# Kernel tuning notes

Hardware: AMD Instinct MI355X
Metric: run time of the kernel (lower is better)

Reference implementation:

```python
import jax, jax.numpy as jnp
import numpy as np

C1 = 256
C2 = 256
C = 256

def setup_inputs() -> dict:
    key = jax.random.key(0)
    ks = jax.random.split(key, 8)
    B, S, H, W = 4, 8, 32, 32
    img_feat = jax.random.normal(ks[0], (B, S, C1, H, W), dtype=jnp.float32)
    depth_feat = jax.random.normal(ks[1], (B, S, C2, H, W), dtype=jnp.float32)
    sq = 1.0 / np.sqrt(C1)
    sk = 1.0 / np.sqrt(C2)
    Wq = jax.random.uniform(ks[2], (C1, C), jnp.float32, -sq, sq)
    bq = jax.random.uniform(ks[3], (C,), jnp.float32, -sq, sq)
    Wk = jax.random.uniform(ks[4], (C2, C), jnp.float32, -sk, sk)
    bk = jax.random.uniform(ks[5], (C,), jnp.float32, -sk, sk)
    Wv = jax.random.uniform(ks[6], (C2, C), jnp.float32, -sk, sk)
    bv = jax.random.uniform(ks[7], (C,), jnp.float32, -sk, sk)
    return {"img_feat": img_feat, "depth_feat": depth_feat,
            "Wq": Wq, "bq": bq, "Wk": Wk, "bk": bk, "Wv": Wv, "bv": bv}

def reference(img_feat, depth_feat, Wq, bq, Wk, bk, Wv, bv):
    B, S, _, H, W = img_feat.shape
    hw = H * W
    # channels-last, flatten spatial: [B,S,hw,c1]
    img = jnp.transpose(img_feat, (0, 1, 3, 4, 2)).reshape(B, S, hw, -1)
    depth = jnp.transpose(depth_feat, (0, 1, 3, 4, 2)).reshape(B, S, hw, -1)
    q = (img @ Wq + bq).astype(jnp.float32)    # [B,S,hw,c]
    k = (depth @ Wk + bk).astype(jnp.float32)  # [B,S,hw,c]
    v = (depth @ Wv + bv).astype(jnp.float32)  # [B,S,hw,c]
    scale = 1.0 / jnp.sqrt(jnp.float32(Wq.shape[1]))
    scores = jnp.einsum('bsqc,bskc->bsqk', q, k) * scale  # [B,S,hw,hw]
    attn = jax.nn.softmax(scores, axis=-1)
    out = jnp.einsum('bsqk,bskc->bsqc', attn, v)          # [B,S,hw,c]
    out = out + img                                        # residual (c == c1)
    out = out.reshape(B, S, H, W, -1).astype(img_feat.dtype)
    return jnp.transpose(out, (0, 1, 4, 2, 3))             # [B,S,c,H,W]
```

## Files before the change

kernel.cpp:

```cpp
#include <hip/hip_runtime.h>
#include <hip/hip_bf16.h>

typedef __hip_bfloat16 bf16;
typedef __attribute__((ext_vector_type(8))) short short8v;
typedef __attribute__((ext_vector_type(4))) float f32x4;

#define NSLICE 32
#define HW     1024
#define CDIM   256
#define KVT    32

__global__ __launch_bounds__(256)
void wt_prep_kernel(const float* __restrict__ Wq, const float* __restrict__ Wk,
                    const float* __restrict__ Wv, bf16* __restrict__ wt)
{
    const int m = blockIdx.x >> 8;
    const int r = blockIdx.x & 255;
    const int tid = threadIdx.x;
    const float* W = (m == 0) ? Wq : (m == 1) ? Wk : Wv;
    const float sc = (m == 0) ? 0.0625f : 1.0f;
    wt[((size_t)m << 16) + (size_t)tid * 256 + r] = __float2bfloat16(W[r * 256 + tid] * sc);
}

__global__ __launch_bounds__(256)
void qkv_mfma_kernel(const float* __restrict__ img, const float* __restrict__ dep,
                     const bf16* __restrict__ wt,
                     const float* __restrict__ bq, const float* __restrict__ bk,
                     const float* __restrict__ bv,
                     bf16* __restrict__ qo, bf16* __restrict__ ko, bf16* __restrict__ vt)
{
    const int bid   = blockIdx.x;
    const int chalf = bid & 1;
    const int tt    = (bid >> 1) & 15;
    const int s     = bid >> 5;
    const int t0    = tt * 64;

    const int tid  = threadIdx.x;
    const int wave = tid >> 6;
    const int lane = tid & 63;
    const int lo16 = lane & 15;
    const int hi4  = lane >> 4;
    const int cw0  = chalf * 128 + wave * 32;

    __shared__ short Ai[64][40];
    __shared__ short Ad[64][40];

    const int so = tid >> 6;
    const int st = tid & 63;

    const float* imgS = img + (size_t)s * CDIM * HW + t0;
    const float* depS = dep + (size_t)s * CDIM * HW + t0;

    const bf16* wtq = wt;
    const bf16* wtk = wt + (1 << 16);
    const bf16* wtv = wt + (2 << 16);

    f32x4 aq[2][4], ak[2][4], av[4][2];
    #pragma unroll
    for (int a = 0; a < 2; ++a)
        #pragma unroll
        for (int b = 0; b < 4; ++b) {
            aq[a][b] = (f32x4){0.f, 0.f, 0.f, 0.f};
            ak[a][b] = (f32x4){0.f, 0.f, 0.f, 0.f};
            av[b][a] = (f32x4){0.f, 0.f, 0.f, 0.f};
        }

    float ri[8], rd[8];
    #pragma unroll
    for (int j = 0; j < 8; ++j) {
        ri[j] = imgS[(size_t)(so * 8 + j) * HW + st];
        rd[j] = depS[(size_t)(so * 8 + j) * HW + st];
    }

    for (int kc = 0; kc < 8; ++kc) {
        __syncthreads();
        {
            short ti[8], td[8];
            #pragma unroll
            for (int j = 0; j < 8; ++j) {
                bf16 hi = __float2bfloat16(ri[j]);
                bf16 hd = __float2bfloat16(rd[j]);
                ti[j] = *reinterpret_cast<short*>(&hi);
                td[j] = *reinterpret_cast<short*>(&hd);
            }
            *reinterpret_cast<short8v*>(&Ai[st][so * 8]) = *reinterpret_cast<short8v*>(ti);
            *reinterpret_cast<short8v*>(&Ad[st][so * 8]) = *reinterpret_cast<short8v*>(td);
        }
        __syncthreads();

        if (kc < 7) {
            #pragma unroll
            for (int j = 0; j < 8; ++j) {
                ri[j] = imgS[(size_t)((kc + 1) * 32 + so * 8 + j) * HW + st];
                rd[j] = depS[(size_t)((kc + 1) * 32 + so * 8 + j) * HW + st];
            }
        }

        short8v xi[4], xd[4];
        #pragma unroll
        for (int nf = 0; nf < 4; ++nf) {
            xi[nf] = *reinterpret_cast<const short8v*>(&Ai[nf * 16 + lo16][hi4 * 8]);
            xd[nf] = *reinterpret_cast<const short8v*>(&Ad[nf * 16 + lo16][hi4 * 8]);
        }
        const int koff = kc * 32 + hi4 * 8;
        short8v wqf[2], wkf[2], wvf[2];
        #pragma unroll
        for (int mf = 0; mf < 2; ++mf) {
            const size_t wrow = (size_t)(cw0 + mf * 16 + lo16) * 256 + koff;
            wqf[mf] = *reinterpret_cast<const short8v*>(wtq + wrow);
            wkf[mf] = *reinterpret_cast<const short8v*>(wtk + wrow);
            wvf[mf] = *reinterpret_cast<const short8v*>(wtv + wrow);
        }

        #pragma unroll
        for (int mf = 0; mf < 2; ++mf)
            #pragma unroll
            for (int nf = 0; nf < 4; ++nf) {
                aq[mf][nf] = __builtin_amdgcn_mfma_f32_16x16x32_bf16(wqf[mf], xi[nf], aq[mf][nf], 0, 0, 0);
                ak[mf][nf] = __builtin_amdgcn_mfma_f32_16x16x32_bf16(wkf[mf], xd[nf], ak[mf][nf], 0, 0, 0);
            }
        #pragma unroll
        for (int mf = 0; mf < 4; ++mf)
            #pragma unroll
            for (int nf = 0; nf < 2; ++nf)
                av[mf][nf] = __builtin_amdgcn_mfma_f32_16x16x32_bf16(xd[mf], wvf[nf], av[mf][nf], 0, 0, 0);
    }

    #pragma unroll
    for (int mf = 0; mf < 2; ++mf) {
        const int cb = cw0 + mf * 16 + 4 * hi4;
        const float4 b4q = *reinterpret_cast<const float4*>(bq + cb);
        const float4 b4k = *reinterpret_cast<const float4*>(bk + cb);
        const float bqa[4] = {b4q.x * 0.0625f, b4q.y * 0.0625f, b4q.z * 0.0625f, b4q.w * 0.0625f};
        const float bka[4] = {b4k.x, b4k.y, b4k.z, b4k.w};
        #pragma unroll
        for (int nf = 0; nf < 4; ++nf) {
            const int tok = t0 + nf * 16 + lo16;
            bf16 tq[4], tk[4];
            #pragma unroll
            for (int g = 0; g < 4; ++g) {
                tq[g] = __float2bfloat16(aq[mf][nf][g] + bqa[g]);
                tk[g] = __float2bfloat16(ak[mf][nf][g] + bka[g]);
            }
            const size_t base = ((size_t)s * HW + tok) * CDIM + cb;
            *reinterpret_cast<uint2*>(&qo[base]) = *reinterpret_cast<uint2*>(tq);
            *reinterpret_cast<uint2*>(&ko[base]) = *reinterpret_cast<uint2*>(tk);
        }
    }
    #pragma unroll
    for (int nf = 0; nf < 2; ++nf) {
        const int c = cw0 + nf * 16 + lo16;
        const float bvv = bv[c];
        #pragma unroll
        for (int mf = 0; mf < 4; ++mf) {
            const int tb = t0 + mf * 16 + 4 * hi4;
            bf16 tv[4];
            #pragma unroll
            for (int g = 0; g < 4; ++g)
                tv[g] = __float2bfloat16(av[mf][nf][g] + bvv);
            *reinterpret_cast<uint2*>(&vt[((size_t)s * CDIM + c) * HW + tb]) =
                *reinterpret_cast<uint2*>(tv);
        }
    }
}

__global__ __launch_bounds__(256)
void flash_mfma_kernel(const bf16* __restrict__ q, const bf16* __restrict__ k,
                       const bf16* __restrict__ vt, const float* __restrict__ img,
                       float* __restrict__ out)
{
    const int bid = blockIdx.x;
    const int qt  = bid >> 5;
    const int rr_ = bid & 31;
    const int s   = (rr_ & 7) * 4 + (rr_ >> 3);
    const int t0  = qt * 64;

    const int tid  = threadIdx.x;
    const int wave = tid >> 6;
    const int lane = tid & 63;
    const int lo16 = lane & 15;
    const int hi4  = lane >> 4;

    __shared__ short Ks[KVT][264];
    __shared__ short Vs[CDIM][36];
    __shared__ short Ps[4][16][36];

    short8v qf[8];
    {
        const int qrow = t0 + wave * 16 + lo16;
        const bf16* qp = q + ((size_t)s * HW + qrow) * CDIM + hi4 * 8;
        #pragma unroll
        for (int kf = 0; kf < 8; ++kf)
            qf[kf] = *reinterpret_cast<const short8v*>(qp + kf * 32);
    }

    f32x4 Oacc[16];
    #pragma unroll
    for (int cf = 0; cf < 16; ++cf) Oacc[cf] = (f32x4){0.f, 0.f, 0.f, 0.f};
    float lp[4] = {0.f, 0.f, 0.f, 0.f};

    const bf16* kS  = k  + (size_t)s * HW * CDIM;
    const bf16* vtS = vt + (size_t)s * CDIM * HW;

    const int krow = tid >> 3;
    const int kch  = tid & 7;
    const int vcl  = lane >> 2;
    const int vtq  = (lane & 3) * 8;

    short8v kreg[4], vreg[4];
    {
        #pragma unroll
        for (int u = 0; u < 4; ++u)
            kreg[u] = *reinterpret_cast<const short8v*>(kS + (size_t)krow * CDIM + (kch + u * 8) * 8);
        #pragma unroll
        for (int u = 0; u < 4; ++u) {
            const int c = wave * 64 + u * 16 + vcl;
            vreg[u] = *reinterpret_cast<const short8v*>(vtS + (size_t)c * HW + vtq);
        }
    }

    for (int kt = 0; kt < HW / KVT; ++kt) {
        __syncthreads();
        #pragma unroll
        for (int u = 0; u < 4; ++u)
            *reinterpret_cast<short8v*>(&Ks[krow][(kch + u * 8) * 8]) = kreg[u];
        #pragma unroll
        for (int u = 0; u < 4; ++u)
            *reinterpret_cast<short8v*>(&Vs[wave * 64 + u * 16 + vcl][vtq]) = vreg[u];
        __syncthreads();

        if (kt + 1 < HW / KVT) {
            const bf16* src = kS + (size_t)(kt + 1) * KVT * CDIM;
            #pragma unroll
            for (int u = 0; u < 4; ++u)
                kreg[u] = *reinterpret_cast<const short8v*>(src + (size_t)krow * CDIM + (kch + u * 8) * 8);
            #pragma unroll
            for (int u = 0; u < 4; ++u) {
                const int c = wave * 64 + u * 16 + vcl;
                vreg[u] = *reinterpret_cast<const short8v*>(vtS + (size_t)c * HW + (kt + 1) * KVT + vtq);
            }
        }

        f32x4 sa[2];
        sa[0] = (f32x4){0.f, 0.f, 0.f, 0.f};
        sa[1] = (f32x4){0.f, 0.f, 0.f, 0.f};
        __builtin_amdgcn_s_setprio(1);
        #pragma unroll
        for (int ks = 0; ks < 8; ++ks) {
            #pragma unroll
            for (int cf = 0; cf < 2; ++cf) {
                short8v bfr = *reinterpret_cast<const short8v*>(
                    &Ks[cf * 16 + lo16][ks * 32 + hi4 * 8]);
                sa[cf] = __builtin_amdgcn_mfma_f32_16x16x32_bf16(qf[ks], bfr, sa[cf], 0, 0, 0);
            }
        }
        __builtin_amdgcn_s_setprio(0);

        #pragma unroll
        for (int cf = 0; cf < 2; ++cf)
            #pragma unroll
            for (int g = 0; g < 4; ++g) {
                const float e = __expf(sa[cf][g]);
                lp[g] += e;
                bf16 hb = __float2bfloat16(e);
                Ps[wave][4 * hi4 + g][cf * 16 + lo16] = *reinterpret_cast<short*>(&hb);
            }

        const short8v pa = *reinterpret_cast<const short8v*>(&Ps[wave][lo16][hi4 * 8]);

        __builtin_amdgcn_s_setprio(1);
        #pragma unroll
        for (int cf = 0; cf < 16; ++cf) {
            const short8v vb = *reinterpret_cast<const short8v*>(&Vs[cf * 16 + lo16][hi4 * 8]);
            Oacc[cf] = __builtin_amdgcn_mfma_f32_16x16x32_bf16(pa, vb, Oacc[cf], 0, 0, 0);
        }
        __builtin_amdgcn_s_setprio(0);
    }

    float inv[4];
    #pragma unroll
    for (int g = 0; g < 4; ++g) {
        float l = lp[g];
        #pragma unroll
        for (int off = 1; off < 16; off <<= 1) l += __shfl_xor(l, off);
        inv[g] = 1.0f / l;
    }
    const float* imgS = img + (size_t)s * CDIM * HW;
    float*       outS = out + (size_t)s * CDIM * HW;
    const int tt = t0 + wave * 16 + 4 * hi4;
    #pragma unroll
    for (int cf = 0; cf < 16; ++cf) {
        const int c = cf * 16 + lo16;
        const float4 r4 = *reinterpret_cast<const float4*>(imgS + (size_t)c * HW + tt);
        float4 o;
        o.x = Oacc[cf][0] * inv[0] + r4.x;
        o.y = Oacc[cf][1] * inv[1] + r4.y;
        o.z = Oacc[cf][2] * inv[2] + r4.z;
        o.w = Oacc[cf][3] * inv[3] + r4.w;
        *reinterpret_cast<float4*>(outS + (size_t)c * HW + tt) = o;
    }
}

extern "C" void kernel_launch(void* const* d_in, const int* in_sizes, int n_in,
                              void* d_out, int out_size, void* d_ws, size_t ws_size,
                              hipStream_t stream)
{
    const float* img = (const float*)d_in[0];
    const float* dep = (const float*)d_in[1];
    const float* Wq  = (const float*)d_in[2];
    const float* bq  = (const float*)d_in[3];
    const float* Wk  = (const float*)d_in[4];
    const float* bk  = (const float*)d_in[5];
    const float* Wv  = (const float*)d_in[6];
    const float* bv  = (const float*)d_in[7];
    float* out = (float*)d_out;

    const size_t npt  = (size_t)NSLICE * HW * CDIM;
    const size_t need = 3 * npt * sizeof(bf16) + 3 * 65536 * sizeof(bf16);
    if (ws_size < need) {
        hipMemsetAsync(d_out, 0, (size_t)out_size * sizeof(float), stream);
        return;
    }

    bf16* q  = (bf16*)d_ws;
    bf16* k  = q + npt;
    bf16* vt = k + npt;
    bf16* wt = vt + npt;

    wt_prep_kernel<<<dim3(3 * 256), 256, 0, stream>>>(Wq, Wk, Wv, wt);

    qkv_mfma_kernel<<<dim3(NSLICE * 32), 256, 0, stream>>>(
        img, dep, wt, bq, bk, bv, q, k, vt);

    flash_mfma_kernel<<<dim3(NSLICE * 16), 256, 0, stream>>>(q, k, vt, img, out);
}
```

Before: 134.1 us.

## Split QKV projection into Q and KV kernels and swizzle flash LDS tiles

The fused QKV projection kernel is split into a Q-only kernel and a K/V kernel. Both use a block-index mapping that interleaves slices across blocks. In the flash kernel, the padded K, V and P shared-memory arrays are replaced with unpadded, XOR-swizzled layouts. The V tile load also changes so each thread reads one full channel row. The aim is to reduce register pressure in the projection and to avoid LDS bank conflicts while cutting LDS footprint, at the cost of an extra kernel launch and more complex swizzle indexing.

```diff
diff --git a/kernel.cpp b/kernel.cpp
--- a/kernel.cpp
+++ b/kernel.cpp
@@ -23,16 +23,13 @@
 }
 
 __global__ __launch_bounds__(256)
-void qkv_mfma_kernel(const float* __restrict__ img, const float* __restrict__ dep,
-                     const bf16* __restrict__ wt,
-                     const float* __restrict__ bq, const float* __restrict__ bk,
-                     const float* __restrict__ bv,
-                     bf16* __restrict__ qo, bf16* __restrict__ ko, bf16* __restrict__ vt)
+void proj_q_kernel(const float* __restrict__ img, const bf16* __restrict__ wt,
+                   const float* __restrict__ bq, bf16* __restrict__ qo)
 {
     const int bid   = blockIdx.x;
-    const int chalf = bid & 1;
-    const int tt    = (bid >> 1) & 15;
-    const int s     = bid >> 5;
+    const int s     = (bid & 7) * 4 + ((bid >> 3) & 3);
+    const int tt    = (bid >> 5) & 15;
+    const int chalf = bid >> 9;
     const int t0    = tt * 64;
 
     const int tid  = threadIdx.x;
@@ -43,152 +40,214 @@
     const int cw0  = chalf * 128 + wave * 32;
 
     __shared__ short Ai[64][40];
-    __shared__ short Ad[64][40];
-
-    const int so = tid >> 6;
-    const int st = tid & 63;
-
+
+    const int so = tid >> 6, st = tid & 63;
     const float* imgS = img + (size_t)s * CDIM * HW + t0;
-    const float* depS = dep + (size_t)s * CDIM * HW + t0;
-
-    const bf16* wtq = wt;
-    const bf16* wtk = wt + (1 << 16);
-    const bf16* wtv = wt + (2 << 16);
-
-    f32x4 aq[2][4], ak[2][4], av[4][2];
+
+    f32x4 aq[2][4];
     #pragma unroll
     for (int a = 0; a < 2; ++a)
         #pragma unroll
-        for (int b = 0; b < 4; ++b) {
-            aq[a][b] = (f32x4){0.f, 0.f, 0.f, 0.f};
-            ak[a][b] = (f32x4){0.f, 0.f, 0.f, 0.f};
-            av[b][a] = (f32x4){0.f, 0.f, 0.f, 0.f};
-        }
-
-    float ri[8], rd[8];
-    #pragma unroll
-    for (int j = 0; j < 8; ++j) {
-        ri[j] = imgS[(size_t)(so * 8 + j) * HW + st];
-        rd[j] = depS[(size_t)(so * 8 + j) * HW + st];
-    }
+        for (int b = 0; b < 4; ++b) aq[a][b] = (f32x4){0.f, 0.f, 0.f, 0.f};
+
+    float ri[8];
+    #pragma unroll
+    for (int j = 0; j < 8; ++j) ri[j] = imgS[(size_t)(so * 8 + j) * HW + st];
 
     for (int kc = 0; kc < 8; ++kc) {
         __syncthreads();
         {
-            short ti[8], td[8];
+            short ti[8];
             #pragma unroll
             for (int j = 0; j < 8; ++j) {
-                bf16 hi = __float2bfloat16(ri[j]);
-                bf16 hd = __float2bfloat16(rd[j]);
-                ti[j] = *reinterpret_cast<short*>(&hi);
-                td[j] = *reinterpret_cast<short*>(&hd);
+                bf16 hb = __float2bfloat16(ri[j]);
+                ti[j] = *reinterpret_cast<short*>(&hb);
             }
             *reinterpret_cast<short8v*>(&Ai[st][so * 8]) = *reinterpret_cast<short8v*>(ti);
-            *reinterpret_cast<short8v*>(&Ad[st][so * 8]) = *reinterpret_cast<short8v*>(td);
         }
         __syncthreads();
 
         if (kc < 7) {
             #pragma unroll
-            for (int j = 0; j < 8; ++j) {
+            for (int j = 0; j < 8; ++j)
                 ri[j] = imgS[(size_t)((kc + 1) * 32 + so * 8 + j) * HW + st];
-                rd[j] = depS[(size_t)((kc + 1) * 32 + so * 8 + j) * HW + st];
-            }
-        }
-
-        short8v xi[4], xd[4];
-        #pragma unroll
-        for (int nf = 0; nf < 4; ++nf) {
+        }
+
+        short8v xi[4];
+        #pragma unroll
+        for (int nf = 0; nf < 4; ++nf)
             xi[nf] = *reinterpret_cast<const short8v*>(&Ai[nf * 16 + lo16][hi4 * 8]);
-            xd[nf] = *reinterpret_cast<const short8v*>(&Ad[nf * 16 + lo16][hi4 * 8]);
-        }
+
         const int koff = kc * 32 + hi4 * 8;
-        short8v wqf[2], wkf[2], wvf[2];
-        #pragma unroll
-        for (int mf = 0; mf < 2; ++mf) {
-            const size_t wrow = (size_t)(cw0 + mf * 16 + lo16) * 256 + koff;
-            wqf[mf] = *reinterpret_cast<const short8v*>(wtq + wrow);
-            wkf[mf] = *reinterpret_cast<const short8v*>(wtk + wrow);
-            wvf[mf] = *reinterpret_cast<const short8v*>(wtv + wrow);
-        }
-
+        short8v wqf[2];
         #pragma unroll
         for (int mf = 0; mf < 2; ++mf)
-            #pragma unroll
-            for (int nf = 0; nf < 4; ++nf) {
+            wqf[mf] = *reinterpret_cast<const short8v*>(
+                wt + (size_t)(cw0 + mf * 16 + lo16) * 256 + koff);
+
+        #pragma unroll
+        for (int mf = 0; mf < 2; ++mf)
+            #pragma unroll
+            for (int nf = 0; nf < 4; ++nf)
                 aq[mf][nf] = __builtin_amdgcn_mfma_f32_16x16x32_bf16(wqf[mf], xi[nf], aq[mf][nf], 0, 0, 0);
-                ak[mf][nf] = __builtin_amdgcn_mfma_f32_16x16x32_bf16(wkf[mf], xd[nf], ak[mf][nf], 0, 0, 0);
-            }
-        #pragma unroll
-        for (int mf = 0; mf < 4; ++mf)
-            #pragma unroll
-            for (int nf = 0; nf < 2; ++nf)
-                av[mf][nf] = __builtin_amdgcn_mfma_f32_16x16x32_bf16(xd[mf], wvf[nf], av[mf][nf], 0, 0, 0);
     }
 
     #pragma unroll
     for (int mf = 0; mf < 2; ++mf) {
         const int cb = cw0 + mf * 16 + 4 * hi4;
-        const float4 b4q = *reinterpret_cast<const float4*>(bq + cb);
-        const float4 b4k = *reinterpret_cast<const float4*>(bk + cb);
-        const float bqa[4] = {b4q.x * 0.0625f, b4q.y * 0.0625f, b4q.z * 0.0625f, b4q.w * 0.0625f};
-        const float bka[4] = {b4k.x, b4k.y, b4k.z, b4k.w};
+        const float4 b4 = *reinterpret_cast<const float4*>(bq + cb);
+        const float ba[4] = {b4.x * 0.0625f, b4.y * 0.0625f, b4.z * 0.0625f, b4.w * 0.0625f};
         #pragma unroll
         for (int nf = 0; nf < 4; ++nf) {
             const int tok = t0 + nf * 16 + lo16;
-            bf16 tq[4], tk[4];
-            #pragma unroll
-            for (int g = 0; g < 4; ++g) {
-                tq[g] = __float2bfloat16(aq[mf][nf][g] + bqa[g]);
-                tk[g] = __float2bfloat16(ak[mf][nf][g] + bka[g]);
-            }
-            const size_t base = ((size_t)s * HW + tok) * CDIM + cb;
-            *reinterpret_cast<uint2*>(&qo[base]) = *reinterpret_cast<uint2*>(tq);
-            *reinterpret_cast<uint2*>(&ko[base]) = *reinterpret_cast<uint2*>(tk);
-        }
-    }
-    #pragma unroll
-    for (int nf = 0; nf < 2; ++nf) {
-        const int c = cw0 + nf * 16 + lo16;
-        const float bvv = bv[c];
-        #pragma unroll
-        for (int mf = 0; mf < 4; ++mf) {
-            const int tb = t0 + mf * 16 + 4 * hi4;
-            bf16 tv[4];
+            bf16 tq[4];
             #pragma unroll
             for (int g = 0; g < 4; ++g)
-                tv[g] = __float2bfloat16(av[mf][nf][g] + bvv);
-            *reinterpret_cast<uint2*>(&vt[((size_t)s * CDIM + c) * HW + tb]) =
-                *reinterpret_cast<uint2*>(tv);
+                tq[g] = __float2bfloat16(aq[mf][nf][g] + ba[g]);
+            *reinterpret_cast<uint2*>(&qo[((size_t)s * HW + tok) * CDIM + cb]) =
+                *reinterpret_cast<uint2*>(tq);
         }
     }
 }
 
 __global__ __launch_bounds__(256)
-void flash_mfma_kernel(const bf16* __restrict__ q, const bf16* __restrict__ k,
-                       const bf16* __restrict__ vt, const float* __restrict__ img,
-                       float* __restrict__ out)
-{
-    const int bid = blockIdx.x;
-    const int qt  = bid >> 5;
-    const int rr_ = bid & 31;
-    const int s   = (rr_ & 7) * 4 + (rr_ >> 3);
-    const int t0  = qt * 64;
+void proj_kv_kernel(const float* __restrict__ dep, const bf16* __restrict__ wt,
+                    const float* __restrict__ bk, const float* __restrict__ bv,
+                    bf16* __restrict__ ko, bf16* __restrict__ vt)
+{
+    const int bid   = blockIdx.x;
+    const int s     = (bid & 7) * 4 + ((bid >> 3) & 3);
+    const int tt    = (bid >> 5) & 15;
+    const int chalf = bid >> 9;
+    const int t0    = tt * 64;
 
     const int tid  = threadIdx.x;
     const int wave = tid >> 6;
     const int lane = tid & 63;
     const int lo16 = lane & 15;
     const int hi4  = lane >> 4;
-
-    __shared__ short Ks[KVT][264];
-    __shared__ short Vs[CDIM][36];
-    __shared__ short Ps[4][16][36];
+    const int cw0  = chalf * 128 + wave * 32;
+
+    __shared__ short Ad[64][40];
+
+    const int so = tid >> 6, st = tid & 63;
+    const float* depS = dep + (size_t)s * CDIM * HW + t0;
+    const bf16* wtk = wt + (1 << 16);
+    const bf16* wtv = wt + (2 << 16);
+
+    f32x4 ak[2][4], av[4][2];
+    #pragma unroll
+    for (int a = 0; a < 2; ++a)
+        #pragma unroll
+        for (int b = 0; b < 4; ++b) {
+            ak[a][b] = (f32x4){0.f, 0.f, 0.f, 0.f};
+            av[b][a] = (f32x4){0.f, 0.f, 0.f, 0.f};
+        }
+
+    float rd[8];
+    #pragma unroll
+    for (int j = 0; j < 8; ++j) rd[j] = depS[(size_t)(so * 8 + j) * HW + st];
+
+    for (int kc = 0; kc < 8; ++kc) {
+        __syncthreads();
+        {
+            short td[8];
+            #pragma unroll
+            for (int j = 0; j < 8; ++j) {
+                bf16 hb = __float2bfloat16(rd[j]);
+                td[j] = *reinterpret_cast<short*>(&hb);
+            }
+            *reinterpret_cast<short8v*>(&Ad[st][so * 8]) = *reinterpret_cast<short8v*>(td);
+        }
+        __syncthreads();
+
+        if (kc < 7) {
+            #pragma unroll
+            for (int j = 0; j < 8; ++j)
+                rd[j] = depS[(size_t)((kc + 1) * 32 + so * 8 + j) * HW + st];
+        }
+
+        short8v xd[4];
+        #pragma unroll
+        for (int nf = 0; nf < 4; ++nf)
+            xd[nf] = *reinterpret_cast<const short8v*>(&Ad[nf * 16 + lo16][hi4 * 8]);
+
+        const int koff = kc * 32 + hi4 * 8;
+        short8v wkf[2], wvf[2];
+        #pragma unroll
+        for (int mf = 0; mf < 2; ++mf) {
+            const size_t wrow = (size_t)(cw0 + mf * 16 + lo16) * 256 + koff;
+            wkf[mf] = *reinterpret_cast<const short8v*>(wtk + wrow);
+            wvf[mf] = *reinterpret_cast<const short8v*>(wtv + wrow);
+        }
+
+        #pragma unroll
+        for (int mf = 0; mf < 2; ++mf)
+            #pragma unroll
+            for (int nf = 0; nf < 4; ++nf)
+                ak[mf][nf] = __builtin_amdgcn_mfma_f32_16x16x32_bf16(wkf[mf], xd[nf], ak[mf][nf], 0, 0, 0);
+        #pragma unroll
+        for (int mf = 0; mf < 4; ++mf)
+            #pragma unroll
+            for (int nf = 0; nf < 2; ++nf)
+                av[mf][nf] = __builtin_amdgcn_mfma_f32_16x16x32_bf16(xd[mf], wvf[nf], av[mf][nf], 0, 0, 0);
+    }
+
+    #pragma unroll
+    for (int mf = 0; mf < 2; ++mf) {
+        const int cb = cw0 + mf * 16 + 4 * hi4;
+        const float4 b4 = *reinterpret_cast<const float4*>(bk + cb);
+        const float ba[4] = {b4.x, b4.y, b4.z, b4.w};
+        #pragma unroll
+        for (int nf = 0; nf < 4; ++nf) {
+            const int tok = t0 + nf * 16 + lo16;
+            bf16 tk[4];
+            #pragma unroll
+            for (int g = 0; g < 4; ++g)
+                tk[g] = __float2bfloat16(ak[mf][nf][g] + ba[g]);
+            *reinterpret_cast<uint2*>(&ko[((size_t)s * HW + tok) * CDIM + cb]) =
+                *reinterpret_cast<uint2*>(tk);
+        }
+    }
+    #pragma unroll
+    for (int nf = 0; nf < 2; ++nf) {
+        const int c = cw0 + nf * 16 + lo16;
+        const float bvv = bv[c];
+        #pragma unroll
+        for (int mf = 0; mf < 4; ++mf) {
+            const int tb = t0 + mf * 16 + 4 * hi4;
+            bf16 tv[4];
+            #pragma unroll
+            for (int g = 0; g < 4; ++g)
+                tv[g] = __float2bfloat16(av[mf][nf][g] + bvv);
+            *reinterpret_cast<uint2*>(&vt[((size_t)s * CDIM + c) * HW + tb]) =
+                *reinterpret_cast<uint2*>(tv);
+        }
+    }
+}
+
+__global__ __launch_bounds__(256)
+void flash_mfma_kernel(const bf16* __restrict__ q, const bf16* __restrict__ k,
+                       const bf16* __restrict__ vt, const float* __restrict__ img,
+                       float* __restrict__ out)
+{
+    const int bid = blockIdx.x;
+    const int s   = (bid & 7) * 4 + ((bid >> 3) & 3);
+    const int t0  = (bid >> 5) * 64;
+
+    const int tid  = threadIdx.x;
+    const int wave = tid >> 6;
+    const int lane = tid & 63;
+    const int lo16 = lane & 15;
+    const int hi4  = lane >> 4;
+
+    __shared__ short KsL[32 * 256];
+    __shared__ short VsL[256 * 32];
+    __shared__ short PsL[4 * 16 * 32];
 
     short8v qf[8];
     {
-        const int qrow = t0 + wave * 16 + lo16;
-        const bf16* qp = q + ((size_t)s * HW + qrow) * CDIM + hi4 * 8;
+        const bf16* qp = q + ((size_t)s * HW + t0 + wave * 16 + lo16) * CDIM + hi4 * 8;
         #pragma unroll
         for (int kf = 0; kf < 8; ++kf)
             qf[kf] = *reinterpret_cast<const short8v*>(qp + kf * 32);
@@ -204,40 +263,33 @@
 
     const int krow = tid >> 3;
     const int kch  = tid & 7;
-    const int vcl  = lane >> 2;
-    const int vtq  = (lane & 3) * 8;
+    const int kxor = krow & 7;
+    const int vxor = (tid >> 1) & 3;
 
     short8v kreg[4], vreg[4];
-    {
+    #pragma unroll
+    for (int u = 0; u < 4; ++u) {
+        kreg[u] = *reinterpret_cast<const short8v*>(kS + (size_t)krow * CDIM + (kch + 8 * u) * 8);
+        vreg[u] = *reinterpret_cast<const short8v*>(vtS + (size_t)tid * HW + u * 8);
+    }
+
+    const int pvRow = lo16 * 32 + (hi4 ^ ((lo16 >> 1) & 3)) * 8;
+    for (int kt = 0; kt < HW / KVT; ++kt) {
+        __syncthreads();
         #pragma unroll
         for (int u = 0; u < 4; ++u)
-            kreg[u] = *reinterpret_cast<const short8v*>(kS + (size_t)krow * CDIM + (kch + u * 8) * 8);
-        #pragma unroll
-        for (int u = 0; u < 4; ++u) {
-            const int c = wave * 64 + u * 16 + vcl;
-            vreg[u] = *reinterpret_cast<const short8v*>(vtS + (size_t)c * HW + vtq);
-        }
-    }
-
-    for (int kt = 0; kt < HW / KVT; ++kt) {
-        __syncthreads();
+            *reinterpret_cast<short8v*>(&KsL[krow * 256 + ((kch ^ kxor) + 8 * u) * 8]) = kreg[u];
         #pragma unroll
         for (int u = 0; u < 4; ++u)
-            *reinterpret_cast<short8v*>(&Ks[krow][(kch + u * 8) * 8]) = kreg[u];
-        #pragma unroll
-        for (int u = 0; u < 4; ++u)
-            *reinterpret_cast<short8v*>(&Vs[wave * 64 + u * 16 + vcl][vtq]) = vreg[u];
+            *reinterpret_cast<short8v*>(&VsL[tid * 32 + (u ^ vxor) * 8]) = vreg[u];
         __syncthreads();
 
         if (kt + 1 < HW / KVT) {
             const bf16* src = kS + (size_t)(kt + 1) * KVT * CDIM;
             #pragma unroll
-            for (int u = 0; u < 4; ++u)
-                kreg[u] = *reinterpret_cast<const short8v*>(src + (size_t)krow * CDIM + (kch + u * 8) * 8);
-            #pragma unroll
             for (int u = 0; u < 4; ++u) {
-                const int c = wave * 64 + u * 16 + vcl;
-                vreg[u] = *reinterpret_cast<const short8v*>(vtS + (size_t)c * HW + (kt + 1) * KVT + vtq);
+                kreg[u] = *reinterpret_cast<const short8v*>(src + (size_t)krow * CDIM + (kch + 8 * u) * 8);
+                vreg[u] = *reinterpret_cast<const short8v*>(vtS + (size_t)tid * HW + (kt + 1) * KVT + u * 8);
             }
         }
 
@@ -249,8 +301,9 @@
         for (int ks = 0; ks < 8; ++ks) {
             #pragma unroll
             for (int cf = 0; cf < 2; ++cf) {
+                const int row = cf * 16 + lo16;
                 short8v bfr = *reinterpret_cast<const short8v*>(
-                    &Ks[cf * 16 + lo16][ks * 32 + hi4 * 8]);
+                    &KsL[row * 256 + ((4 * ks + hi4) ^ (lo16 & 7)) * 8]);
                 sa[cf] = __builtin_amdgcn_mfma_f32_16x16x32_bf16(qf[ks], bfr, sa[cf], 0, 0, 0);
             }
         }
@@ -263,15 +316,19 @@
                 const float e = __expf(sa[cf][g]);
                 lp[g] += e;
                 bf16 hb = __float2bfloat16(e);
-                Ps[wave][4 * hi4 + g][cf * 16 + lo16] = *reinterpret_cast<short*>(&hb);
-            }
-
-        const short8v pa = *reinterpret_cast<const short8v*>(&Ps[wave][lo16][hi4 * 8]);
+                const int r = 4 * hi4 + g;
+                const int ch = (2 * cf + (lo16 >> 3)) ^ ((r >> 1) & 3);
+                PsL[wave * 512 + r * 32 + ch * 8 + (lo16 & 7)] = *reinterpret_cast<short*>(&hb);
+            }
+
+        const short8v pa = *reinterpret_cast<const short8v*>(&PsL[wave * 512 + pvRow]);
 
         __builtin_amdgcn_s_setprio(1);
         #pragma unroll
         for (int cf = 0; cf < 16; ++cf) {
-            const short8v vb = *reinterpret_cast<const short8v*>(&Vs[cf * 16 + lo16][hi4 * 8]);
+            const int row = cf * 16 + lo16;
+            const short8v vb = *reinterpret_cast<const short8v*>(
+                &VsL[row * 32 + (hi4 ^ ((lo16 >> 1) & 3)) * 8]);
             Oacc[cf] = __builtin_amdgcn_mfma_f32_16x16x32_bf16(pa, vb, Oacc[cf], 0, 0, 0);
         }
         __builtin_amdgcn_s_setprio(0);
@@ -329,8 +386,8 @@
 
     wt_prep_kernel<<<dim3(3 * 256), 256, 0, stream>>>(Wq, Wk, Wv, wt);
 
-    qkv_mfma_kernel<<<dim3(NSLICE * 32), 256, 0, stream>>>(
-        img, dep, wt, bq, bk, bv, q, k, vt);
+    proj_q_kernel<<<dim3(NSLICE * 32), 256, 0, stream>>>(img, wt, bq, q);
+    proj_kv_kernel<<<dim3(NSLICE * 32), 256, 0, stream>>>(dep, wt, bk, bv, k, vt);
 
     flash_mfma_kernel<<<dim3(NSLICE * 16), 256, 0, stream>>>(q, k, vt, img, out);
 }
```

Measured after the change: 123.0 us. 8.3% less time.
